# Optimization experiments

Measured on AMD Instinct MI355X. Metric: run time of the kernel, lower is better.

Reference implementation:

```python
import jax, jax.numpy as jnp
import numpy as np

EPS = 1e-12
RANK = 16


def setup_inputs() -> dict:
    key = jax.random.key(0)
    ks = jax.random.split(key, 7)
    bs, seq, d_in, d_out = 8, 2048, 4096, 4096
    n_tasks, n_splits, n_skills, rank = 256, 1, 8, RANK
    return {
        "x": jax.random.normal(ks[0], (bs, seq, d_in), dtype=jnp.float32),
        "task_ids": jax.random.randint(ks[1], (bs,), 0, n_tasks, dtype=jnp.int64 if jax.config.jax_enable_x64 else jnp.int32),
        "weight": jax.random.normal(ks[2], (d_out, d_in), dtype=jnp.float32) * 0.02,
        "bias": jax.random.normal(ks[3], (d_out,), dtype=jnp.float32) * 0.02,
        "module_logits": jax.random.normal(ks[4], (n_tasks, n_splits * n_skills), dtype=jnp.float32) * 0.001,
        "lora_a": jax.random.normal(ks[5], (n_splits, n_skills, d_in // n_splits, rank), dtype=jnp.float32) * 0.01,
        "lora_b": jax.random.normal(ks[6], (n_splits, n_skills, rank, d_out // n_splits), dtype=jnp.float32) * 0.01,
    }


def reference(x, task_ids, weight, bias, module_logits, lora_a, lora_b):
    bs = x.shape[0]
    n_splits, n_skills, _, rank = lora_a.shape
    d_in = n_splits * lora_a.shape[2]
    d_out = n_splits * lora_b.shape[3]
    # PolytroponSelector (eval path): sigmoid then sum-normalize over skills
    logits = module_logits[task_ids].reshape(bs, n_splits, n_skills)
    mw = jax.nn.sigmoid(logits)
    mw = mw / (mw.sum(axis=-1, keepdims=True) + EPS)  # [b, q, s]
    # Mix LoRA skill matrices per example
    A = jnp.einsum('bqs,qsdr->bqdr', mw, lora_a).reshape(bs, d_in, rank)
    B = jnp.einsum('bqs,qsrd->bqrd', mw, lora_b)
    B = jnp.transpose(B, (0, 2, 1, 3)).reshape(bs, rank, d_out)
    adapter_out = jnp.einsum('btr,brd->btd', jnp.einsum('bti,bir->btr', x, A), B) / rank
    base = jnp.einsum('bti,oi->bto', x, weight) + bias
    return base + adapter_out
```

## Files before the change

### kernel.cpp

```cpp
#include <hip/hip_runtime.h>
#include <hip/hip_bf16.h>
#include <cstdint>
#include <cstddef>

typedef __bf16 bf16_t;
typedef __bf16 bf16x8 __attribute__((ext_vector_type(8)));
typedef float f32x4 __attribute__((ext_vector_type(4)));

#define GLP(p)  (const __attribute__((address_space(1))) void*)(p)
#define LDSP(p) (__attribute__((address_space(3))) void*)(p)

static constexpr int BS   = 8;
static constexpr int SEQ  = 2048;
static constexpr int DIN  = 4096;
static constexpr int DOUT = 4096;
static constexpr int NSK  = 8;
static constexpr int RANK = 16;
static constexpr int MTOT = BS * SEQ;

static __device__ __forceinline__ bf16x8 cvt8(float4 v0, float4 v1) {
    bf16x8 o;
    o[0] = (bf16_t)v0.x; o[1] = (bf16_t)v0.y; o[2] = (bf16_t)v0.z; o[3] = (bf16_t)v0.w;
    o[4] = (bf16_t)v1.x; o[5] = (bf16_t)v1.y; o[6] = (bf16_t)v1.z; o[7] = (bf16_t)v1.w;
    return o;
}

__global__ __launch_bounds__(256) void mix_kernel(
    const float* __restrict__ logits, const int* __restrict__ task_ids,
    const float* __restrict__ lora_a, const float* __restrict__ lora_b,
    bf16_t* __restrict__ Abt, bf16_t* __restrict__ Btp) {
    int b = blockIdx.y;
    int c = blockIdx.x;
    int tid = threadIdx.x;

    int t = task_ids[b];
    float w[NSK]; float sum = 0.f;
#pragma unroll
    for (int s = 0; s < NSK; ++s) {
        float lg = logits[t * NSK + s];
        float sg = 1.f / (1.f + __expf(-lg));
        w[s] = sg; sum += sg;
    }
    float inv = 1.f / (sum + 1e-12f);
#pragma unroll
    for (int s = 0; s < NSK; ++s) w[s] *= inv;

    {
        int r = tid & 15, kk = tid >> 4;
#pragma unroll
        for (int i = 0; i < 4; ++i) {
            int k = c * 64 + i * 16 + kk;
            float acc = 0.f;
#pragma unroll
            for (int s = 0; s < NSK; ++s)
                acc += w[s] * lora_a[((size_t)s * DIN + k) * RANK + r];
            Abt[((size_t)b * RANK + r) * DIN + k] = (bf16_t)acc;
        }
    }
    {
        int n = c * 64 + (tid & 63);
        int r0 = tid >> 6;
#pragma unroll
        for (int i = 0; i < 4; ++i) {
            int rr = r0 + i * 4;
            float acc = 0.f;
#pragma unroll
            for (int s = 0; s < NSK; ++s)
                acc += w[s] * lora_b[((size_t)s * RANK + rr) * DOUT + n];
            Btp[((size_t)b * DOUT + n) * 32 + rr] = (bf16_t)acc;
            Btp[((size_t)b * DOUT + n) * 32 + 16 + rr] = (bf16_t)0.f;
        }
    }
}

__global__ __launch_bounds__(256) void convw_kernel(const float* __restrict__ W,
                                                    bf16_t* __restrict__ Wb) {
    size_t g = (size_t)blockIdx.x * 256 + threadIdx.x;
    const float4* src = (const float4*)W;
    float4 v0 = src[g * 2], v1 = src[g * 2 + 1];
    *(bf16x8*)(Wb + g * 8) = cvt8(v0, v1);
}

template<bool XPRE>
__global__ __launch_bounds__(256) void tconv_kernel(
    const float* __restrict__ x, const bf16_t* __restrict__ Abt,
    bf16_t* __restrict__ xb, bf16_t* __restrict__ tpad) {
    __shared__ __align__(16) bf16_t As[64 * 64];
    __shared__ __align__(16) bf16_t Aa[16 * 64];

    int row0 = blockIdx.x * 64;
    int b = row0 >> 11;
    int tid = threadIdx.x;
    int w = tid >> 6, l = tid & 63;
    const bf16_t* Ab = Abt + (size_t)b * RANK * DIN;

    f32x4 acc = {0.f, 0.f, 0.f, 0.f};

    for (int k0 = 0; k0 < DIN; k0 += 64) {
#pragma unroll
        for (int i = 0; i < 2; ++i) {
            int flat = i * 256 + tid;
            int row = flat >> 3, c8 = flat & 7;
            const float* src = x + (size_t)(row0 + row) * DIN + k0 + c8 * 8;
            float4 v0 = *(const float4*)src;
            float4 v1 = *(const float4*)(src + 4);
            bf16x8 o = cvt8(v0, v1);
            *(bf16x8*)(&As[flat * 8]) = o;
            if (XPRE)
                *(bf16x8*)(xb + (size_t)(row0 + row) * DIN + k0 + c8 * 8) = o;
        }
        if (tid < 128) {
            int r = tid >> 3, c8 = tid & 7;
            __builtin_amdgcn_global_load_lds(GLP(Ab + (size_t)r * DIN + k0 + c8 * 8),
                                             LDSP(&Aa[tid * 8]), 16, 0, 0);
        }
        __syncthreads();
#pragma unroll
        for (int s = 0; s < 2; ++s) {
            int kr = s * 32 + (l >> 4) * 8;
            bf16x8 a = *(const bf16x8*)(&As[(w * 16 + (l & 15)) * 64 + kr]);
            bf16x8 bb = *(const bf16x8*)(&Aa[(l & 15) * 64 + kr]);
            acc = __builtin_amdgcn_mfma_f32_16x16x32_bf16(a, bb, acc, 0, 0, 0);
        }
        __syncthreads();
    }
    int r = l & 15;
    int rowb = w * 16 + (l >> 4) * 4;
#pragma unroll
    for (int j = 0; j < 4; ++j) {
        int gm = row0 + rowb + j;
        tpad[(size_t)gm * 32 + r] = (bf16_t)(acc[j] * 0.0625f);
        tpad[(size_t)gm * 32 + 16 + r] = (bf16_t)0.f;
    }
}

#define LGKM0  asm volatile("s_waitcnt lgkmcnt(0)" ::: "memory")
#define SBAR   __builtin_amdgcn_s_barrier()
#define SCHEDB __builtin_amdgcn_sched_barrier(0)
#define PRIO1  __builtin_amdgcn_s_setprio(1)
#define PRIO0  __builtin_amdgcn_s_setprio(0)
#define VMG(TXT) asm volatile("s_waitcnt " TXT ::: "memory")

#define MFMA_Q(AREG, BREG, QM, QN)                                             \
    _Pragma("unroll") for (int s_ = 0; s_ < 2; ++s_)                           \
    _Pragma("unroll") for (int i_ = 0; i_ < 4; ++i_)                           \
    _Pragma("unroll") for (int jj_ = 0; jj_ < 2; ++jj_)                        \
        acc[(QM)*4 + i_][(QN)*2 + jj_] =                                       \
            __builtin_amdgcn_mfma_f32_16x16x32_bf16(                           \
                AREG[i_][s_], BREG[jj_][s_], acc[(QM)*4 + i_][(QN)*2 + jj_],   \
                0, 0, 0);

#define TILE_BODY(CP, ISS1, ISS2, ISS3, G0TXT, G1TXT, G3TXT)                   \
  {                                                                            \
    const bf16_t* A0s = &lds[CP][0][0];                                        \
    const bf16_t* A1s = &lds[CP][1][0];                                        \
    const bf16_t* B0s = &lds[CP][2][0];                                        \
    const bf16_t* B1s = &lds[CP][3][0];                                        \
    bf16x8 aA[4][2], aB[4][2], bA[2][2], bB[2][2];                             \
                                                 \
    loadA(A0s, aA); loadB(B0s, bA);                                            \
    SCHEDB; SBAR; LGKM0; SCHEDB;                                               \
    PRIO1; MFMA_Q(aA, bA, 0, 0); PRIO0;                                        \
    VMG(G0TXT); SCHEDB; SBAR; SCHEDB;                                          \
                                                 \
    loadB(B1s, bB);                                                            \
    ISS1;                                                                      \
    SCHEDB; SBAR; LGKM0; SCHEDB;                                               \
    PRIO1; MFMA_Q(aA, bB, 0, 1); PRIO0;                                        \
    VMG(G1TXT); SCHEDB; SBAR; SCHEDB;                                          \
                                                 \
    loadA(A1s, aB);                                                            \
    ISS2;                                                                      \
    SCHEDB; SBAR; LGKM0; SCHEDB;                                               \
    PRIO1; MFMA_Q(aB, bB, 1, 1); PRIO0;                                        \
    SCHEDB; SBAR; SCHEDB;                                                      \
                                                 \
    ISS3;                                                                      \
    SCHEDB; SBAR; SCHEDB;                                                      \
    PRIO1; MFMA_Q(aB, bA, 1, 0); PRIO0;                                        \
    VMG(G3TXT); SCHEDB; SBAR; SCHEDB;                                          \
  }

__global__ __launch_bounds__(512, 2) void gemm8_kernel(
    const bf16_t* __restrict__ xb, const bf16_t* __restrict__ Wb,
    const float* __restrict__ bias,
    const bf16_t* __restrict__ tpad, const bf16_t* __restrict__ Btp,
    float* __restrict__ out) {
    __shared__ __align__(16) bf16_t lds[2][4][128 * 64];

    int tid = threadIdx.x;
    int w = tid >> 6, l = tid & 63;
    int wm = w >> 2, wn = w & 3;
    int l4 = l >> 4, l15 = l & 15;

    int orig = blockIdx.x;
    int id = (orig & 7) * 128 + (orig >> 3);
    int mb = id >> 4, nb = id & 15;
    int row0 = mb * 256, col0 = nb * 256;
    int b = row0 >> 11;

    f32x4 acc[8][4] = {};

    auto stageA = [&](int kt, int par, int half) {
        int k0 = kt * 64;
        const bf16_t* src = xb + (size_t)(row0 + half * 128) * DIN;
        bf16_t* dst = &lds[par][half][0];
#pragma unroll
        for (int ld = 0; ld < 2; ++ld) {
            int flat = ld * 512 + tid;
            int r = flat >> 3;
            int sc = (flat & 7) ^ (r & 7);
            __builtin_amdgcn_global_load_lds(
                GLP(src + (size_t)r * DIN + k0 + sc * 8),
                LDSP(dst + flat * 8), 16, 0, 0);
        }
    };
    auto stageB = [&](int kt, int par, int half) {
        int k0 = kt * 64;
        const bf16_t* src = Wb + (size_t)(col0 + half * 128) * DIN;
        bf16_t* dst = &lds[par][2 + half][0];
#pragma unroll
        for (int ld = 0; ld < 2; ++ld) {
            int flat = ld * 512 + tid;
            int r = flat >> 3;
            int sc = (flat & 7) ^ (r & 7);
            __builtin_amdgcn_global_load_lds(
                GLP(src + (size_t)r * DIN + k0 + sc * 8),
                LDSP(dst + flat * 8), 16, 0, 0);
        }
    };
    auto stageAdpA = [&]() {
#pragma unroll
        for (int ld = 0; ld < 2; ++ld) {
            int flat = ld * 512 + tid;
            int r = flat >> 2, c4 = flat & 3;
            __builtin_amdgcn_global_load_lds(
                GLP(tpad + (size_t)(row0 + r) * 32 + c4 * 8),
                LDSP(&lds[0][0][flat * 8]), 16, 0, 0);
        }
    };
    auto stageAdpB = [&]() {
#pragma unroll
        for (int ld = 0; ld < 2; ++ld) {
            int flat = ld * 512 + tid;
            int r = flat >> 2, c4 = flat & 3;
            __builtin_amdgcn_global_load_lds(
                GLP(Btp + ((size_t)b * DOUT + col0 + r) * 32 + c4 * 8),
                LDSP(&lds[0][2][flat * 8]), 16, 0, 0);
        }
    };

    auto loadA = [&](const bf16_t* base, bf16x8 (&ar)[4][2]) {
#pragma unroll
        for (int i = 0; i < 4; ++i) {
            int row = wm * 64 + i * 16 + l15;
#pragma unroll
            for (int s = 0; s < 2; ++s)
                ar[i][s] = *(const bf16x8*)(base + row * 64 +
                                            (((s * 4 + l4) ^ (l15 & 7)) << 3));
        }
    };
    auto loadB = [&](const bf16_t* base, bf16x8 (&br)[2][2]) {
#pragma unroll
        for (int jj = 0; jj < 2; ++jj) {
            int row = wn * 32 + jj * 16 + l15;
#pragma unroll
            for (int s = 0; s < 2; ++s)
                br[jj][s] = *(const bf16x8*)(base + row * 64 +
                                             (((s * 4 + l4) ^ (l15 & 7)) << 3));
        }
    };

    stageA(0, 0, 0); stageB(0, 0, 0); stageB(0, 0, 1); stageA(0, 0, 1);
    stageA(1, 1, 0); stageB(1, 1, 0); stageB(1, 1, 1); stageA(1, 1, 1);
    VMG("vmcnt(12)");
    SCHEDB; SBAR; SCHEDB;

#pragma unroll 1
    for (int j = 0; j < 62; ++j) {
        int cp = j & 1;
        TILE_BODY(cp,
                  { stageA(j + 2, cp, 0); stageB(j + 2, cp, 0); },
                  { stageB(j + 2, cp, 1); },
                  { stageA(j + 2, cp, 1); },
                  "vmcnt(10)", "vmcnt(12)", "vmcnt(12)");
    }
    TILE_BODY(0,
              { stageAdpA(); stageAdpB(); },
              {}, {},
              "vmcnt(10)", "vmcnt(12)", "vmcnt(8)");
    TILE_BODY(1,
              {}, {}, {},
              "vmcnt(6)", "vmcnt(4)", "vmcnt(0)");

    {
        const bf16_t* A0 = &lds[0][0][0];
        const bf16_t* B0 = &lds[0][2][0];
        bf16x8 aa[8]; bf16x8 bb[4];
#pragma unroll
        for (int ai = 0; ai < 8; ++ai) {
            int row = (ai >> 2) * 128 + wm * 64 + (ai & 3) * 16 + l15;
            aa[ai] = *(const bf16x8*)(A0 + row * 32 + l4 * 8);
        }
#pragma unroll
        for (int bj = 0; bj < 4; ++bj) {
            int row = (bj >> 1) * 128 + wn * 32 + (bj & 1) * 16 + l15;
            bb[bj] = *(const bf16x8*)(B0 + row * 32 + l4 * 8);
        }
#pragma unroll
        for (int ai = 0; ai < 8; ++ai)
#pragma unroll
            for (int bj = 0; bj < 4; ++bj)
                acc[ai][bj] = __builtin_amdgcn_mfma_f32_16x16x32_bf16(
                    aa[ai], bb[bj], acc[ai][bj], 0, 0, 0);
    }

#pragma unroll
    for (int ai = 0; ai < 8; ++ai) {
        int gm = row0 + (ai >> 2) * 128 + wm * 64 + (ai & 3) * 16 + l4 * 4;
#pragma unroll
        for (int bj = 0; bj < 4; ++bj) {
            int gn = col0 + (bj >> 1) * 128 + wn * 32 + (bj & 1) * 16 + l15;
            float bsv = bias[gn];
#pragma unroll
            for (int q = 0; q < 4; ++q)
                out[(size_t)(gm + q) * DOUT + gn] = acc[ai][bj][q] + bsv;
        }
    }
}

template<bool WPRE>
__global__ __launch_bounds__(256) void gemm_kernel(
    const float* __restrict__ xf,
    const float* __restrict__ Wf, const bf16_t* __restrict__ Wb,
    const float* __restrict__ bias,
    const bf16_t* __restrict__ tpad, const bf16_t* __restrict__ Btp,
    float* __restrict__ out) {
    __shared__ __align__(16) bf16_t As[128 * 64];
    __shared__ __align__(16) bf16_t Bs[128 * 64];

    int orig = blockIdx.x;
    int id = (orig & 7) * 512 + (orig >> 3);
    int mb = id >> 5, nb = id & 31;
    int row0 = mb * 128, col0 = nb * 128;
    int b = row0 >> 11;

    int tid = threadIdx.x;
    int w = tid >> 6, l = tid & 63;
    int wm = w >> 1, wn = w & 1;

    f32x4 acc[4][4] = {};

    for (int k0 = 0; k0 < DIN; k0 += 64) {
#pragma unroll
        for (int i = 0; i < 4; ++i) {
            int flat = i * 256 + tid;
            int row = flat >> 3, c8 = flat & 7;
            const float* src = xf + (size_t)(row0 + row) * DIN + k0 + c8 * 8;
            float4 v0 = *(const float4*)src;
            float4 v1 = *(const float4*)(src + 4);
            *(bf16x8*)(&As[flat * 8]) = cvt8(v0, v1);
        }
        if constexpr (WPRE) {
#pragma unroll
            for (int i = 0; i < 4; ++i) {
                int flat = i * 256 + tid;
                int row = flat >> 3, c8 = flat & 7;
                __builtin_amdgcn_global_load_lds(
                    GLP(Wb + (size_t)(col0 + row) * DIN + k0 + c8 * 8),
                    LDSP(&Bs[flat * 8]), 16, 0, 0);
            }
        } else {
#pragma unroll
            for (int i = 0; i < 4; ++i) {
                int flat = i * 256 + tid;
                int row = flat >> 3, c8 = flat & 7;
                const float* src = Wf + (size_t)(col0 + row) * DIN + k0 + c8 * 8;
                float4 v0 = *(const float4*)src;
                float4 v1 = *(const float4*)(src + 4);
                *(bf16x8*)(&Bs[flat * 8]) = cvt8(v0, v1);
            }
        }
        __syncthreads();
#pragma unroll
        for (int s = 0; s < 2; ++s) {
            int kr = s * 32 + (l >> 4) * 8;
            bf16x8 a[4], bf[4];
#pragma unroll
            for (int i = 0; i < 4; ++i)
                a[i] = *(const bf16x8*)(&As[(wm * 64 + i * 16 + (l & 15)) * 64 + kr]);
#pragma unroll
            for (int j = 0; j < 4; ++j)
                bf[j] = *(const bf16x8*)(&Bs[(wn * 64 + j * 16 + (l & 15)) * 64 + kr]);
#pragma unroll
            for (int i = 0; i < 4; ++i)
#pragma unroll
                for (int j = 0; j < 4; ++j)
                    acc[i][j] = __builtin_amdgcn_mfma_f32_16x16x32_bf16(a[i], bf[j], acc[i][j], 0, 0, 0);
        }
        __syncthreads();
    }

    {
#pragma unroll
        for (int i = 0; i < 2; ++i) {
            int flat = i * 256 + tid;
            int row = flat >> 2, c8 = flat & 3;
            __builtin_amdgcn_global_load_lds(
                GLP(tpad + (size_t)(row0 + row) * 32 + c8 * 8),
                LDSP(&As[flat * 8]), 16, 0, 0);
            __builtin_amdgcn_global_load_lds(
                GLP(Btp + ((size_t)b * DOUT + col0 + row) * 32 + c8 * 8),
                LDSP(&Bs[flat * 8]), 16, 0, 0);
        }
        __syncthreads();
        int kr = (l >> 4) * 8;
        bf16x8 a[4], bf[4];
#pragma unroll
        for (int i = 0; i < 4; ++i)
            a[i] = *(const bf16x8*)(&As[(wm * 64 + i * 16 + (l & 15)) * 32 + kr]);
#pragma unroll
        for (int j = 0; j < 4; ++j)
            bf[j] = *(const bf16x8*)(&Bs[(wn * 64 + j * 16 + (l & 15)) * 32 + kr]);
#pragma unroll
        for (int i = 0; i < 4; ++i)
#pragma unroll
            for (int j = 0; j < 4; ++j)
                acc[i][j] = __builtin_amdgcn_mfma_f32_16x16x32_bf16(a[i], bf[j], acc[i][j], 0, 0, 0);
    }

#pragma unroll
    for (int i = 0; i < 4; ++i) {
        int gm = row0 + wm * 64 + i * 16 + (l >> 4) * 4;
#pragma unroll
        for (int j = 0; j < 4; ++j) {
            int gn = col0 + wn * 64 + j * 16 + (l & 15);
            float bs = bias[gn];
#pragma unroll
            for (int q = 0; q < 4; ++q)
                out[(size_t)(gm + q) * DOUT + gn] = acc[i][j][q] + bs;
        }
    }
}

extern "C" void kernel_launch(void* const* d_in, const int* in_sizes, int n_in,
                              void* d_out, int out_size, void* d_ws, size_t ws_size,
                              hipStream_t stream) {
    const float* x        = (const float*)d_in[0];
    const int*   task_ids = (const int*)d_in[1];
    const float* W        = (const float*)d_in[2];
    const float* bias     = (const float*)d_in[3];
    const float* logits   = (const float*)d_in[4];
    const float* lora_a   = (const float*)d_in[5];
    const float* lora_b   = (const float*)d_in[6];
    float* out = (float*)d_out;

    char* ws = (char*)d_ws;
    size_t off = 0;
    auto alloc = [&](size_t bytes) {
        char* p = ws + off;
        off += (bytes + 255) & ~(size_t)255;
        return p;
    };
    bf16_t* Abt  = (bf16_t*)alloc((size_t)BS * RANK * DIN * 2);
    bf16_t* Btp  = (bf16_t*)alloc((size_t)BS * DOUT * 32 * 2);
    bf16_t* tpad = (bf16_t*)alloc((size_t)MTOT * 32 * 2);
    bf16_t* Wb   = (bf16_t*)alloc((size_t)DOUT * DIN * 2);
    size_t w_end = off;
    bf16_t* xb   = (bf16_t*)alloc((size_t)MTOT * DIN * 2);
    size_t full_end = off;

    bool wpre = ws_size >= w_end;
    bool xpre = ws_size >= full_end;

    mix_kernel<<<dim3(64, 8), 256, 0, stream>>>(logits, task_ids, lora_a, lora_b, Abt, Btp);
    if (wpre)
        convw_kernel<<<(DOUT * DIN / 8) / 256, 256, 0, stream>>>(W, Wb);
    if (xpre)
        tconv_kernel<true><<<MTOT / 64, 256, 0, stream>>>(x, Abt, xb, tpad);
    else
        tconv_kernel<false><<<MTOT / 64, 256, 0, stream>>>(x, Abt, nullptr, tpad);

    if (xpre) {
        int nblk = (MTOT / 256) * (DOUT / 256);
        gemm8_kernel<<<nblk, 512, 0, stream>>>(xb, Wb, bias, tpad, Btp, out);
    } else {
        int nblk = (MTOT / 128) * (DOUT / 128);
        if (wpre)
            gemm_kernel<true><<<nblk, 256, 0, stream>>>(x, W, Wb, bias, tpad, Btp, out);
        else
            gemm_kernel<false><<<nblk, 256, 0, stream>>>(x, W, Wb, bias, tpad, Btp, out);
    }
}
```

Before: 611.8 us.

## Restructure GEMM main loop into finer-grained staggered LDS/global pipeline

Reworks the 8-wave bf16 GEMM main loop so global-to-LDS staging of the next tile's quarters is interleaved across the four MFMA phases, with per-quarter buffer reuse and partial lgkmcnt waits instead of full drains. The next tile's A fragment is preloaded during the last phase, and the loop is unrolled by two with explicit buffer parities. This aims to hide LDS read latency and reduce barrier stalls. In exchange the vmcnt/lgkmcnt bookkeeping becomes fragile, and a wrong count could introduce races on the reused LDS halves.

Result: slower. 997.4 us (+63.0%).

```diff
diff --git a/kernel.cpp b/kernel.cpp
--- a/kernel.cpp
+++ b/kernel.cpp
@@ -150,35 +150,31 @@
                 AREG[i_][s_], BREG[jj_][s_], acc[(QM)*4 + i_][(QN)*2 + jj_],   \
                 0, 0, 0);
 
-#define TILE_BODY(CP, ISS1, ISS2, ISS3, G0TXT, G1TXT, G3TXT)                   \
+#define TILE_T(P, S0, S1, S2, S3, G0, G2, G3, PH3R)                            \
   {                                                                            \
-    const bf16_t* A0s = &lds[CP][0][0];                                        \
-    const bf16_t* A1s = &lds[CP][1][0];                                        \
-    const bf16_t* B0s = &lds[CP][2][0];                                        \
-    const bf16_t* B1s = &lds[CP][3][0];                                        \
-    bf16x8 aA[4][2], aB[4][2], bA[2][2], bB[2][2];                             \
-                                                 \
-    loadA(A0s, aA); loadB(B0s, bA);                                            \
-    SCHEDB; SBAR; LGKM0; SCHEDB;                                               \
-    PRIO1; MFMA_Q(aA, bA, 0, 0); PRIO0;                                        \
-    VMG(G0TXT); SCHEDB; SBAR; SCHEDB;                                          \
-                                                 \
-    loadB(B1s, bB);                                                            \
-    ISS1;                                                                      \
-    SCHEDB; SBAR; LGKM0; SCHEDB;                                               \
-    PRIO1; MFMA_Q(aA, bB, 0, 1); PRIO0;                                        \
-    VMG(G1TXT); SCHEDB; SBAR; SCHEDB;                                          \
-                                                 \
-    loadA(A1s, aB);                                                            \
-    ISS2;                                                                      \
-    SCHEDB; SBAR; LGKM0; SCHEDB;                                               \
-    PRIO1; MFMA_Q(aB, bB, 1, 1); PRIO0;                                        \
+                                    \
+    loadB(&lds[P][2][0], bA);                                                  \
+    loadB(&lds[P][3][0], bB);                                                  \
+    S0;                                                                        \
+    G0; SCHEDB; SBAR; SCHEDB;                                                  \
+    asm volatile("s_waitcnt lgkmcnt(4)" ::: "memory"); SCHEDB;                 \
+    PRIO1; MFMA_Q(aA, bA, 0, 0); PRIO0; SCHEDB;                                \
+                                       \
+    loadA(&lds[P][1][0], aB);                                                  \
+    S1;                                                                        \
     SCHEDB; SBAR; SCHEDB;                                                      \
-                                                 \
-    ISS3;                                                                      \
-    SCHEDB; SBAR; SCHEDB;                                                      \
-    PRIO1; MFMA_Q(aB, bA, 1, 0); PRIO0;                                        \
-    VMG(G3TXT); SCHEDB; SBAR; SCHEDB;                                          \
+    asm volatile("s_waitcnt lgkmcnt(8)" ::: "memory"); SCHEDB;                 \
+    PRIO1; MFMA_Q(aA, bB, 0, 1); PRIO0; SCHEDB;                                \
+                                                     \
+    S2;                                                                        \
+    G2; SCHEDB; SBAR; SCHEDB;                                                  \
+    LGKM0; SCHEDB;                                                             \
+    PRIO1; MFMA_Q(aB, bB, 1, 1); PRIO0; SCHEDB;                                \
+                                  \
+    PH3R;                                                                      \
+    S3;                                                                        \
+    G3; SCHEDB; SBAR; SCHEDB;                                                  \
+    PRIO1; MFMA_Q(aB, bA, 1, 0); PRIO0; SCHEDB;                                \
   }
 
 __global__ __launch_bounds__(512, 2) void gemm8_kernel(
@@ -200,6 +196,7 @@
     int b = row0 >> 11;
 
     f32x4 acc[8][4] = {};
+    bf16x8 aA[4][2], aB[4][2], bA[2][2], bB[2][2];
 
     auto stageA = [&](int kt, int par, int half) {
         int k0 = kt * 64;
@@ -271,28 +268,41 @@
         }
     };
 
-    stageA(0, 0, 0); stageB(0, 0, 0); stageB(0, 0, 1); stageA(0, 0, 1);
-    stageA(1, 1, 0); stageB(1, 1, 0); stageB(1, 1, 1); stageA(1, 1, 1);
-    VMG("vmcnt(12)");
+    stageA(0, 0, 0);
+    stageB(0, 0, 0);
+    stageB(0, 0, 1);
+    stageA(0, 0, 1);
+    stageA(1, 1, 0);
+    stageB(1, 1, 0);
+    VMG("vmcnt(6)");
     SCHEDB; SBAR; SCHEDB;
+    loadA(&lds[0][0][0], aA);
 
 #pragma unroll 1
-    for (int j = 0; j < 62; ++j) {
-        int cp = j & 1;
-        TILE_BODY(cp,
-                  { stageA(j + 2, cp, 0); stageB(j + 2, cp, 0); },
-                  { stageB(j + 2, cp, 1); },
-                  { stageA(j + 2, cp, 1); },
-                  "vmcnt(10)", "vmcnt(12)", "vmcnt(12)");
-    }
-    TILE_BODY(0,
-              { stageAdpA(); stageAdpB(); },
-              {}, {},
-              "vmcnt(10)", "vmcnt(12)", "vmcnt(8)");
-    TILE_BODY(1,
-              {}, {}, {},
-              "vmcnt(6)", "vmcnt(4)", "vmcnt(0)");
-
+    for (int jj = 0; jj < 31; ++jj) {
+        int t0 = jj * 2, t1 = t0 + 1;
+        TILE_T(0,
+               stageB(t0 + 1, 1, 1), stageA(t0 + 1, 1, 1),
+               stageA(t0 + 2, 0, 0), stageB(t0 + 2, 0, 0),
+               VMG("vmcnt(6)"), VMG("vmcnt(8)"), VMG("vmcnt(6)"),
+               loadA(&lds[1][0][0], aA));
+        TILE_T(1,
+               stageB(t1 + 1, 0, 1), stageA(t1 + 1, 0, 1),
+               stageA(t1 + 2, 1, 0), stageB(t1 + 2, 1, 0),
+               VMG("vmcnt(6)"), VMG("vmcnt(8)"), VMG("vmcnt(6)"),
+               loadA(&lds[0][0][0], aA));
+    }
+    TILE_T(0,
+           stageB(63, 1, 1), stageA(63, 1, 1),
+           stageAdpA(), stageAdpB(),
+           VMG("vmcnt(6)"), VMG("vmcnt(8)"), VMG("vmcnt(6)"),
+           loadA(&lds[1][0][0], aA));
+    TILE_T(1,
+           , , , ,
+           VMG("vmcnt(4)"), , ,
+           );
+
+    VMG("vmcnt(0)"); SCHEDB; SBAR; SCHEDB;
     {
         const bf16_t* A0 = &lds[0][0][0];
         const bf16_t* B0 = &lds[0][2][0];
@@ -307,6 +317,7 @@
             int row = (bj >> 1) * 128 + wn * 32 + (bj & 1) * 16 + l15;
             bb[bj] = *(const bf16x8*)(B0 + row * 32 + l4 * 8);
         }
+        LGKM0; SCHEDB;
 #pragma unroll
         for (int ai = 0; ai < 8; ++ai)
 #pragma unroll
```
